# Kernel optimization log

Measured on AMD Instinct MI355X. Metric: run time of the kernel, lower is better.

The kernel has to match this reference:

```python
import jax, jax.numpy as jnp
import numpy as np

N_RES = 20000
N_EDGE = 640000
NUM_RBF = 16
NUM_POS = 16
NUM_AA = 21  # 20 + 1 (unknown)
D_MIN, D_MAX = 2.0, 22.0
EPS = 1e-8


def _quat_to_rot(q):
    # q = (w, x, y, z), assumed normalized
    w, x, y, z = q[..., 0], q[..., 1], q[..., 2], q[..., 3]
    r0 = jnp.stack([1 - 2 * (y * y + z * z), 2 * (x * y - w * z), 2 * (x * z + w * y)], -1)
    r1 = jnp.stack([2 * (x * y + w * z), 1 - 2 * (x * x + z * z), 2 * (y * z - w * x)], -1)
    r2 = jnp.stack([2 * (x * z - w * y), 2 * (y * z + w * x), 1 - 2 * (x * x + y * y)], -1)
    return jnp.stack([r0, r1, r2], -2)  # (..., 3, 3)


def _ideal_virtual_cb(bb):
    # bb: (N, 3, 3) with atoms N, CA, C
    n, ca, c = bb[..., 0, :], bb[..., 1, :], bb[..., 2, :]
    b = ca - n
    cc = c - ca
    a = jnp.cross(b, cc)
    return -0.58273431 * a + 0.56802827 * b - 0.54067466 * cc + ca


def _rbf(D):
    mu = jnp.linspace(D_MIN, D_MAX, NUM_RBF)  # (16,)
    sigma = (D_MAX - D_MIN) / NUM_RBF
    return jnp.exp(-(((D[..., None] - mu) / sigma) ** 2))


def setup_inputs() -> dict:
    key = jax.random.key(0)
    k1, k2, k3, k4, k5, k6 = jax.random.split(key, 6)
    atom14 = jax.random.normal(k1, (N_RES, 14, 3), jnp.float32) * 3.0
    quat = jax.random.normal(k2, (N_RES, 4), jnp.float32)
    quat = quat / jnp.linalg.norm(quat, axis=-1, keepdims=True)
    trans = jax.random.normal(k3, (N_RES, 3), jnp.float32) * 3.0
    rigids7 = jnp.concatenate([quat, trans], axis=-1)  # (N, 7)
    seq = jax.random.randint(k4, (N_RES,), 0, NUM_AA).astype(jnp.int32)
    noising_mask = jax.random.bernoulli(k5, 0.5, (N_RES,))
    edge_index = jax.random.randint(k6, (2, N_EDGE), 0, N_RES)
    return dict(atom14=atom14, rigids7=rigids7, seq=seq,
                noising_mask=noising_mask, edge_index=edge_index)


def reference(atom14, rigids7, seq, noising_mask, edge_index):
    dst, src = edge_index[0], edge_index[1]
    noised_src = noising_mask[src]
    noised_dst = noising_mask[dst]
    keep_src = (~noised_src)[:, None].astype(jnp.float32)
    keep_dst = (~noised_dst)[:, None].astype(jnp.float32)

    feats = [noised_dst.astype(jnp.float32)[:, None],
             noised_src.astype(jnp.float32)[:, None]]

    src_seq = jax.nn.one_hot(seq[src], NUM_AA, dtype=jnp.float32)
    dst_seq = jax.nn.one_hot(seq[dst], NUM_AA, dtype=jnp.float32)
    feats += [src_seq * keep_src, dst_seq * keep_dst]

    bb3 = atom14[:, :3, :]                      # N, CA, C
    cb = _ideal_virtual_cb(bb3)
    bb = jnp.concatenate([bb3, cb[:, None, :]], axis=1)  # (N, 4, 3)

    edge_bb_src = bb[src]                       # (E, 4, 3)
    edge_bb_dst = bb[dst]                       # (E, 4, 3)
    # pairwise distances between 4 backbone atoms of src and dst: (E, 4, 4)
    dists = jnp.linalg.norm(
        edge_bb_src[:, :, None, :] - edge_bb_dst[:, None, :, :] + EPS, axis=-1)
    feats.append(_rbf(dists).reshape(dists.shape[0], -1))  # (E, 256)

    # positional embedding of sequence separation
    d = (dst - src).astype(jnp.float32)
    freq = jnp.exp(jnp.arange(0, NUM_POS, 2, dtype=jnp.float32)
                   * (-np.log(10000.0) / NUM_POS))
    angles = d[:, None] * freq
    feats.append(jnp.concatenate([jnp.cos(angles), jnp.sin(angles)], axis=-1))

    # rigid frames: quaternion + translation; invert_apply = R^T (p - t)
    quat = rigids7[:, :4]
    quat = quat / jnp.linalg.norm(quat, axis=-1, keepdims=True)
    R = _quat_to_rot(quat)                      # (N, 3, 3)
    t = rigids7[:, 4:]                          # (N, 3)

    local = jnp.einsum('nji,nkj->nki', R, bb - t[:, None, :])  # (N, 4, 3)
    src_bb_local = local[src].reshape(-1, 12)

    Rs, ts = R[src], t[src]
    dst_in_src = jnp.einsum('eji,ekj->eki', Rs,
                            edge_bb_dst - ts[:, None, :]).reshape(-1, 12)

    feats += [src_bb_local * keep_src, dst_in_src * keep_dst]
    return jnp.concatenate(feats, axis=-1)  # (E, 340)
```

## Files before the change

### kernel.cpp

```cpp
#include <hip/hip_runtime.h>

#define N_RES   20000
#define N_EDGE  640000
#define NFEAT   340

__device__ __constant__ float c_freq[8] = {
    1.0f, 0.31622776601683794f, 0.1f, 0.031622776601683794f,
    0.01f, 0.0031622776601683794f, 0.001f, 0.00031622776601683794f};

extern "C" __global__ __launch_bounds__(256)
void residue_prep(const float* __restrict__ atom14,
                  const float* __restrict__ rigids7,
                  float* __restrict__ res) {
    int r = blockIdx.x * 256 + threadIdx.x;
    if (r >= N_RES) return;

    const float* a = atom14 + (size_t)r * 42;
    float nx  = a[0], ny  = a[1], nz  = a[2];
    float cax = a[3], cay = a[4], caz = a[5];
    float cx  = a[6], cy  = a[7], cz  = a[8];

    float bx = cax - nx, by = cay - ny, bz = caz - nz;
    float ex = cx - cax, ey = cy - cay, ez = cz - caz;
    float ax = by * ez - bz * ey;
    float ay = bz * ex - bx * ez;
    float az = bx * ey - by * ex;
    float cbx = -0.58273431f * ax + 0.56802827f * bx - 0.54067466f * ex + cax;
    float cby = -0.58273431f * ay + 0.56802827f * by - 0.54067466f * ey + cay;
    float cbz = -0.58273431f * az + 0.56802827f * bz - 0.54067466f * ez + caz;

    const float* q7 = rigids7 + (size_t)r * 7;
    float qw = q7[0], qx = q7[1], qy = q7[2], qz = q7[3];
    float inv = 1.0f / sqrtf(qw * qw + qx * qx + qy * qy + qz * qz);
    qw *= inv; qx *= inv; qy *= inv; qz *= inv;
    float tx = q7[4], ty = q7[5], tz = q7[6];

    float R[9];
    R[0] = 1.0f - 2.0f * (qy * qy + qz * qz);
    R[1] = 2.0f * (qx * qy - qw * qz);
    R[2] = 2.0f * (qx * qz + qw * qy);
    R[3] = 2.0f * (qx * qy + qw * qz);
    R[4] = 1.0f - 2.0f * (qx * qx + qz * qz);
    R[5] = 2.0f * (qy * qz - qw * qx);
    R[6] = 2.0f * (qx * qz - qw * qy);
    R[7] = 2.0f * (qy * qz + qw * qx);
    R[8] = 1.0f - 2.0f * (qx * qx + qy * qy);

    float bb[12] = {nx, ny, nz, cax, cay, caz, cx, cy, cz, cbx, cby, cbz};

    float* o = res + (size_t)r * 36;
    #pragma unroll
    for (int k = 0; k < 12; ++k) o[k] = bb[k];
    #pragma unroll
    for (int k = 0; k < 4; ++k) {
        float x0 = bb[k * 3 + 0] - tx;
        float x1 = bb[k * 3 + 1] - ty;
        float x2 = bb[k * 3 + 2] - tz;
        #pragma unroll
        for (int i = 0; i < 3; ++i)
            o[12 + k * 3 + i] = R[i] * x0 + R[3 + i] * x1 + R[6 + i] * x2;
    }
    #pragma unroll
    for (int j = 0; j < 9; ++j) o[24 + j] = R[j];
    o[33] = tx; o[34] = ty; o[35] = tz;
}

extern "C" __global__ __launch_bounds__(256)
void pos_table(float* __restrict__ tab) {
    int idx = blockIdx.x * 256 + threadIdx.x;
    int row = idx >> 4;
    int m = idx & 15;
    float d = (float)(row - 19999);
    float ang = d * c_freq[m & 7];
    tab[idx] = (m < 8) ? cosf(ang) : sinf(ang);
}

extern "C" __global__ __launch_bounds__(256)
void edge_feats(const int* __restrict__ eidx,
                const int* __restrict__ seq,
                const int* __restrict__ mask,
                const float* __restrict__ res,
                const float* __restrict__ postab,
                float* __restrict__ out) {
    int lane = threadIdx.x & 63;
    int wave = threadIdx.x >> 6;
    int e = __builtin_amdgcn_readfirstlane((int)(blockIdx.x * 4 + wave));

    int dst = eidx[e];
    int src = eidx[N_EDGE + e];
    int msrc = mask[src];
    int mdst = mask[dst];
    float noised_src = msrc ? 1.0f : 0.0f;
    float noised_dst = mdst ? 1.0f : 0.0f;
    float keep_src = 1.0f - noised_src;
    float keep_dst = 1.0f - noised_dst;
    int ssrc = seq[src];
    int sdst = seq[dst];

    const float* rs = res + (size_t)src * 36;
    const float* rd = res + (size_t)dst * 36;
    float* op = out + (size_t)e * NFEAT;

    {
        int ai = lane >> 4;
        int aj = (lane >> 2) & 3;
        const float* sp = rs + ai * 3;
        const float* dp = rd + aj * 3;
        float dx = sp[0] - dp[0] + 1e-8f;
        float dy = sp[1] - dp[1] + 1e-8f;
        float dz = sp[2] - dp[2] + 1e-8f;
        float D = sqrtf(dx * dx + dy * dy + dz * dz);

        int rbase = (lane & 3) * 4;
        float4 v;
        float x;
        float mu;
        mu = 2.0f + (20.0f / 15.0f) * (float)(rbase + 0);
        x = (D - mu) * 0.8f;  v.x = __expf(-x * x);
        mu = 2.0f + (20.0f / 15.0f) * (float)(rbase + 1);
        x = (D - mu) * 0.8f;  v.y = __expf(-x * x);
        mu = 2.0f + (20.0f / 15.0f) * (float)(rbase + 2);
        x = (D - mu) * 0.8f;  v.z = __expf(-x * x);
        mu = 2.0f + (20.0f / 15.0f) * (float)(rbase + 3);
        x = (D - mu) * 0.8f;  v.w = __expf(-x * x);

        *reinterpret_cast<float4*>(op + 44 + 4 * lane) = v;
    }

    if (lane < 44) {
        float v = (lane < 23) ? ((ssrc == lane - 2) ? keep_src : 0.0f)
                              : ((sdst == lane - 23) ? keep_dst : 0.0f);
        if (lane == 0) v = noised_dst;
        if (lane == 1) v = noised_src;
        op[lane] = v;
    } else if (lane < 56) {
        int qq = lane - 44;
        int k = qq / 3;
        int i2 = qq - k * 3;
        float t0 = rs[33], t1 = rs[34], t2 = rs[35];
        float x0 = rd[k * 3 + 0] - t0;
        float x1 = rd[k * 3 + 1] - t1;
        float x2 = rd[k * 3 + 2] - t2;
        float v = (rs[24 + i2] * x0 + rs[27 + i2] * x1 + rs[30 + i2] * x2) * keep_dst;
        op[328 + qq] = v;
    } else if (lane < 60) {
        int c = lane - 56;
        const float4 v = *reinterpret_cast<const float4*>(
            postab + ((size_t)(dst - src + 19999) * 16 + c * 4));
        *reinterpret_cast<float4*>(op + 300 + 4 * c) = v;
    } else if (lane < 63) {
        int c = lane - 60;
        float4 v = *reinterpret_cast<const float4*>(rs + 12 + 4 * c);
        v.x *= keep_src; v.y *= keep_src; v.z *= keep_src; v.w *= keep_src;
        *reinterpret_cast<float4*>(op + 316 + 4 * c) = v;
    }
}

extern "C" void kernel_launch(void* const* d_in, const int* in_sizes, int n_in,
                              void* d_out, int out_size, void* d_ws, size_t ws_size,
                              hipStream_t stream) {
    const float* atom14  = (const float*)d_in[0];
    const float* rigids7 = (const float*)d_in[1];
    const int* seq  = (const int*)d_in[2];
    const int* mask = (const int*)d_in[3];
    const int* eidx = (const int*)d_in[4];
    float* res = (float*)d_ws;
    float* tab = res + 720000;

    hipLaunchKernelGGL(residue_prep, dim3((N_RES + 255) / 256), dim3(256), 0, stream,
                       atom14, rigids7, res);
    hipLaunchKernelGGL(pos_table, dim3(2500), dim3(256), 0, stream, tab);
    hipLaunchKernelGGL(edge_feats, dim3(N_EDGE / 4), dim3(256), 0, stream,
                       eidx, seq, mask, res, tab, (float*)d_out);
}
```

Baseline: 1.010 ms.

## Stage per-edge residue data in shared memory and process 16 edges per block

Each block now cooperatively gathers the src/dst residue records, positional-table rows, sequence and mask values for 16 edges into LDS using float4 loads. Each wave then loops over 4 edges and computes the features from LDS instead of issuing many scattered scalar global loads per edge. The aim is to cut gather latency and the number of global load instructions. The cost is a block-wide barrier and fewer blocks in flight.

```diff
diff --git a/kernel.cpp b/kernel.cpp
--- a/kernel.cpp
+++ b/kernel.cpp
@@ -3,6 +3,7 @@
 #define N_RES   20000
 #define N_EDGE  640000
 #define NFEAT   340
+#define EPB     16
 
 __device__ __constant__ float c_freq[8] = {
     1.0f, 0.31622776601683794f, 0.1f, 0.031622776601683794f,
@@ -82,77 +83,102 @@
                 const float* __restrict__ res,
                 const float* __restrict__ postab,
                 float* __restrict__ out) {
-    int lane = threadIdx.x & 63;
-    int wave = threadIdx.x >> 6;
-    int e = __builtin_amdgcn_readfirstlane((int)(blockIdx.x * 4 + wave));
-
-    int dst = eidx[e];
-    int src = eidx[N_EDGE + e];
-    int msrc = mask[src];
-    int mdst = mask[dst];
-    float noised_src = msrc ? 1.0f : 0.0f;
-    float noised_dst = mdst ? 1.0f : 0.0f;
-    float keep_src = 1.0f - noised_src;
-    float keep_dst = 1.0f - noised_dst;
-    int ssrc = seq[src];
-    int sdst = seq[dst];
-
-    const float* rs = res + (size_t)src * 36;
-    const float* rd = res + (size_t)dst * 36;
-    float* op = out + (size_t)e * NFEAT;
-
-    {
-        int ai = lane >> 4;
-        int aj = (lane >> 2) & 3;
-        const float* sp = rs + ai * 3;
-        const float* dp = rd + aj * 3;
-        float dx = sp[0] - dp[0] + 1e-8f;
-        float dy = sp[1] - dp[1] + 1e-8f;
-        float dz = sp[2] - dp[2] + 1e-8f;
-        float D = sqrtf(dx * dx + dy * dy + dz * dz);
-
-        int rbase = (lane & 3) * 4;
-        float4 v;
-        float x;
-        float mu;
-        mu = 2.0f + (20.0f / 15.0f) * (float)(rbase + 0);
-        x = (D - mu) * 0.8f;  v.x = __expf(-x * x);
-        mu = 2.0f + (20.0f / 15.0f) * (float)(rbase + 1);
-        x = (D - mu) * 0.8f;  v.y = __expf(-x * x);
-        mu = 2.0f + (20.0f / 15.0f) * (float)(rbase + 2);
-        x = (D - mu) * 0.8f;  v.z = __expf(-x * x);
-        mu = 2.0f + (20.0f / 15.0f) * (float)(rbase + 3);
-        x = (D - mu) * 0.8f;  v.w = __expf(-x * x);
-
-        *reinterpret_cast<float4*>(op + 44 + 4 * lane) = v;
+    __shared__ __align__(16) float sm[EPB * 64];
+    __shared__ int s_sd[EPB], s_ss[EPB], s_md[EPB], s_ms[EPB];
+
+    int tid = threadIdx.x;
+    int ebase = blockIdx.x * EPB;
+    int el = tid >> 4;
+    int c  = tid & 15;
+
+    int rdst = eidx[ebase + el];
+    int rsrc = eidx[N_EDGE + ebase + el];
+
+    const float* gp;
+    int loff;
+    if (c < 9)       { gp = res + (size_t)rsrc * 36 + c * 4;                         loff = c * 4; }
+    else if (c < 12) { gp = res + (size_t)rdst * 36 + (c - 9) * 4;                   loff = 36 + (c - 9) * 4; }
+    else             { gp = postab + (size_t)(rdst - rsrc + 19999) * 16 + (c - 12) * 4; loff = 48 + (c - 12) * 4; }
+    float4 gv = *reinterpret_cast<const float4*>(gp);
+    *reinterpret_cast<float4*>(&sm[el * 64 + loff]) = gv;
+
+    if (tid < 64) {
+        int q = tid >> 4, e2 = tid & 15;
+        int idx = (q & 1) ? eidx[N_EDGE + ebase + e2] : eidx[ebase + e2];
+        int v = (q < 2) ? seq[idx] : mask[idx];
+        if (q == 0) s_sd[e2] = v;
+        else if (q == 1) s_ss[e2] = v;
+        else if (q == 2) s_md[e2] = v;
+        else s_ms[e2] = v;
     }
-
-    if (lane < 44) {
-        float v = (lane < 23) ? ((ssrc == lane - 2) ? keep_src : 0.0f)
-                              : ((sdst == lane - 23) ? keep_dst : 0.0f);
-        if (lane == 0) v = noised_dst;
-        if (lane == 1) v = noised_src;
-        op[lane] = v;
-    } else if (lane < 56) {
-        int qq = lane - 44;
-        int k = qq / 3;
-        int i2 = qq - k * 3;
-        float t0 = rs[33], t1 = rs[34], t2 = rs[35];
-        float x0 = rd[k * 3 + 0] - t0;
-        float x1 = rd[k * 3 + 1] - t1;
-        float x2 = rd[k * 3 + 2] - t2;
-        float v = (rs[24 + i2] * x0 + rs[27 + i2] * x1 + rs[30 + i2] * x2) * keep_dst;
-        op[328 + qq] = v;
-    } else if (lane < 60) {
-        int c = lane - 56;
-        const float4 v = *reinterpret_cast<const float4*>(
-            postab + ((size_t)(dst - src + 19999) * 16 + c * 4));
-        *reinterpret_cast<float4*>(op + 300 + 4 * c) = v;
-    } else if (lane < 63) {
-        int c = lane - 60;
-        float4 v = *reinterpret_cast<const float4*>(rs + 12 + 4 * c);
-        v.x *= keep_src; v.y *= keep_src; v.z *= keep_src; v.w *= keep_src;
-        *reinterpret_cast<float4*>(op + 316 + 4 * c) = v;
+    __syncthreads();
+
+    int lane = tid & 63;
+    int wave = tid >> 6;
+
+    #pragma unroll
+    for (int i = 0; i < 4; ++i) {
+        int eloc = wave * 4 + i;
+        int e = ebase + eloc;
+        const float* L = sm + eloc * 64;
+        int ssrc = s_ss[eloc];
+        int sdst = s_sd[eloc];
+        float noised_src = s_ms[eloc] ? 1.0f : 0.0f;
+        float noised_dst = s_md[eloc] ? 1.0f : 0.0f;
+        float keep_src = 1.0f - noised_src;
+        float keep_dst = 1.0f - noised_dst;
+        float* op = out + (size_t)e * NFEAT;
+
+        {
+            int ai = lane >> 4;
+            int aj = (lane >> 2) & 3;
+            float sx = L[ai * 3 + 0], sy = L[ai * 3 + 1], sz = L[ai * 3 + 2];
+            float px = L[36 + aj * 3 + 0], py = L[36 + aj * 3 + 1], pz = L[36 + aj * 3 + 2];
+            float dx = sx - px + 1e-8f;
+            float dy = sy - py + 1e-8f;
+            float dz = sz - pz + 1e-8f;
+            float D = sqrtf(dx * dx + dy * dy + dz * dz);
+
+            int rbase = (lane & 3) * 4;
+            float4 v;
+            float x, mu;
+            mu = 2.0f + (20.0f / 15.0f) * (float)(rbase + 0);
+            x = (D - mu) * 0.8f;  v.x = __expf(-x * x);
+            mu = 2.0f + (20.0f / 15.0f) * (float)(rbase + 1);
+            x = (D - mu) * 0.8f;  v.y = __expf(-x * x);
+            mu = 2.0f + (20.0f / 15.0f) * (float)(rbase + 2);
+            x = (D - mu) * 0.8f;  v.z = __expf(-x * x);
+            mu = 2.0f + (20.0f / 15.0f) * (float)(rbase + 3);
+            x = (D - mu) * 0.8f;  v.w = __expf(-x * x);
+
+            *reinterpret_cast<float4*>(op + 44 + 4 * lane) = v;
+        }
+
+        if (lane < 44) {
+            float v = (lane < 23) ? ((ssrc == lane - 2) ? keep_src : 0.0f)
+                                  : ((sdst == lane - 23) ? keep_dst : 0.0f);
+            if (lane == 0) v = noised_dst;
+            if (lane == 1) v = noised_src;
+            op[lane] = v;
+        } else if (lane < 56) {
+            int qq = lane - 44;
+            int k = qq / 3;
+            int i2 = qq - k * 3;
+            float x0 = L[36 + k * 3 + 0] - L[33];
+            float x1 = L[36 + k * 3 + 1] - L[34];
+            float x2 = L[36 + k * 3 + 2] - L[35];
+            float v = (L[24 + i2] * x0 + L[27 + i2] * x1 + L[30 + i2] * x2) * keep_dst;
+            op[328 + qq] = v;
+        } else if (lane < 60) {
+            int cc = lane - 56;
+            float4 pt = *reinterpret_cast<const float4*>(&L[48 + 4 * cc]);
+            *reinterpret_cast<float4*>(op + 300 + 4 * cc) = pt;
+        } else if (lane < 63) {
+            int cc = lane - 60;
+            float4 sl = *reinterpret_cast<const float4*>(&L[12 + 4 * cc]);
+            sl.x *= keep_src; sl.y *= keep_src; sl.z *= keep_src; sl.w *= keep_src;
+            *reinterpret_cast<float4*>(op + 316 + 4 * cc) = sl;
+        }
     }
 }
 
@@ -170,6 +196,6 @@
     hipLaunchKernelGGL(residue_prep, dim3((N_RES + 255) / 256), dim3(256), 0, stream,
                        atom14, rigids7, res);
     hipLaunchKernelGGL(pos_table, dim3(2500), dim3(256), 0, stream, tab);
-    hipLaunchKernelGGL(edge_feats, dim3(N_EDGE / 4), dim3(256), 0, stream,
+    hipLaunchKernelGGL(edge_feats, dim3(N_EDGE / EPB), dim3(256), 0, stream,
                        eidx, seq, mask, res, tab, (float*)d_out);
 }
```

New measurement: 931.6 us. -7.8%, faster.
